# Kernel tuning notes

Measured on AMD Instinct MI355X. Metric: run time of the kernel, lower is better.

Reference implementation:

```python
import jax, jax.numpy as jnp
import numpy as np

B = 2097152  # number of Gaussians


def setup_inputs() -> dict:
    key = jax.random.key(0)
    k1, k2, k3, k4, k5, k6 = jax.random.split(key, 6)
    return {
        "loc1": jax.random.normal(k1, (B, 3), dtype=jnp.float32),
        "scale1": jax.random.uniform(k2, (B, 3), dtype=jnp.float32),
        "rot_matrix1": jax.random.normal(k3, (B, 3, 3), dtype=jnp.float32),
        "loc2": jax.random.normal(k4, (B, 3), dtype=jnp.float32),
        "scale2": jax.random.uniform(k5, (B, 3), dtype=jnp.float32),
        "rot_matrix2": jax.random.normal(k6, (B, 3, 3), dtype=jnp.float32),
    }


def reference(loc1, scale1, rot_matrix1, loc2, scale2, rot_matrix2):
    # ||mu1 - mu2||^2  -> (B,)
    loc_diff2 = jnp.sum((loc1 - loc2) ** 2, axis=-1)

    # cov2 = R2 diag(scale2) R2^T  -> (B,3,3)
    cov2 = jnp.einsum("bij,bj,bkj->bik", rot_matrix2, scale2, rot_matrix2)
    # cov2 rotated into frame of Gaussian 1: R1^T cov2 R1  -> (B,3,3)
    cov2_R1 = jnp.einsum("bji,bjk,bkl->bil", rot_matrix1, cov2, rot_matrix1)

    # E = diag(sqrt(s1)) cov2_R1 diag(sqrt(s1)), then symmetrize
    s1_sqrt = jnp.sqrt(scale1)  # (B,3)
    E = s1_sqrt[:, :, None] * cov2_R1 * s1_sqrt[:, None, :]
    E = (E + jnp.swapaxes(E, 1, 2)) * 0.5

    # trace of matrix sqrt via eigenvalues: sum (lambda^2)^(1/4) = sum |lambda|^(1/2)
    E_eig = jnp.linalg.eigvalsh(E)  # (B,3)
    E_sqrt_trace = jnp.sum(jnp.sqrt(jnp.sqrt(E_eig ** 2)), axis=-1)

    cov_wasserstein = jnp.sum(scale1, axis=-1) + jnp.sum(scale2, axis=-1) - 2.0 * E_sqrt_trace
    cov_wasserstein = jnp.maximum(cov_wasserstein, 0.0)
    return jnp.sqrt(loc_diff2 + cov_wasserstein)
```

## Files before the change

kernel.cpp:

```cpp
#include <hip/hip_runtime.h>
#include <math.h>

#define BLK  256
#define GRID 2048

struct F3 { float x, y, z; };

__device__ __forceinline__ F3 ldF3(const float* p) {
    F3 r; r.x = p[0]; r.y = p[1]; r.z = p[2]; return r;
}

__device__ __forceinline__ float compute_elem(
    const F3 L1, const F3 L2, const F3 S1, const F3 S2,
    const F3 r1a, const F3 r1b, const F3 r1c,
    const F3 r2a, const F3 r2b, const F3 r2c)
{
    const float dx = L1.x - L2.x, dy = L1.y - L2.y, dz = L1.z - L2.z;
    const float loc_diff2 = dx * dx + dy * dy + dz * dz;

    const float s1a = S1.x, s1b = S1.y, s1c = S1.z;
    const float s2a = S2.x, s2b = S2.y, s2c = S2.z;

    const float R1[9] = {r1a.x, r1a.y, r1a.z, r1b.x, r1b.y, r1b.z, r1c.x, r1c.y, r1c.z};
    const float R2[9] = {r2a.x, r2a.y, r2a.z, r2b.x, r2b.y, r2b.z, r2c.x, r2c.y, r2c.z};

    const float m00 = s2a * R2[0] * R2[0] + s2b * R2[1] * R2[1] + s2c * R2[2] * R2[2];
    const float m01 = s2a * R2[0] * R2[3] + s2b * R2[1] * R2[4] + s2c * R2[2] * R2[5];
    const float m02 = s2a * R2[0] * R2[6] + s2b * R2[1] * R2[7] + s2c * R2[2] * R2[8];
    const float m11 = s2a * R2[3] * R2[3] + s2b * R2[4] * R2[4] + s2c * R2[5] * R2[5];
    const float m12 = s2a * R2[3] * R2[6] + s2b * R2[4] * R2[7] + s2c * R2[5] * R2[8];
    const float m22 = s2a * R2[6] * R2[6] + s2b * R2[7] * R2[7] + s2c * R2[8] * R2[8];

    float A[9];
    A[0] = m00 * R1[0] + m01 * R1[3] + m02 * R1[6];
    A[1] = m00 * R1[1] + m01 * R1[4] + m02 * R1[7];
    A[2] = m00 * R1[2] + m01 * R1[5] + m02 * R1[8];
    A[3] = m01 * R1[0] + m11 * R1[3] + m12 * R1[6];
    A[4] = m01 * R1[1] + m11 * R1[4] + m12 * R1[7];
    A[5] = m01 * R1[2] + m11 * R1[5] + m12 * R1[8];
    A[6] = m02 * R1[0] + m12 * R1[3] + m22 * R1[6];
    A[7] = m02 * R1[1] + m12 * R1[4] + m22 * R1[7];
    A[8] = m02 * R1[2] + m12 * R1[5] + m22 * R1[8];

    float T[9];
    T[0] = R1[0] * A[0] + R1[3] * A[3] + R1[6] * A[6];
    T[1] = R1[0] * A[1] + R1[3] * A[4] + R1[6] * A[7];
    T[2] = R1[0] * A[2] + R1[3] * A[5] + R1[6] * A[8];
    T[3] = R1[1] * A[0] + R1[4] * A[3] + R1[7] * A[6];
    T[4] = R1[1] * A[1] + R1[4] * A[4] + R1[7] * A[7];
    T[5] = R1[1] * A[2] + R1[4] * A[5] + R1[7] * A[8];
    T[6] = R1[2] * A[0] + R1[5] * A[3] + R1[8] * A[6];
    T[7] = R1[2] * A[1] + R1[5] * A[4] + R1[8] * A[7];
    T[8] = R1[2] * A[2] + R1[5] * A[5] + R1[8] * A[8];

    const float sq0 = __builtin_amdgcn_sqrtf(s1a);
    const float sq1 = __builtin_amdgcn_sqrtf(s1b);
    const float sq2 = __builtin_amdgcn_sqrtf(s1c);
    const float e00 = s1a * T[0];
    const float e11 = s1b * T[4];
    const float e22 = s1c * T[8];
    const float e01 = 0.5f * sq0 * sq1 * (T[1] + T[3]);
    const float e02 = 0.5f * sq0 * sq2 * (T[2] + T[6]);
    const float e12 = 0.5f * sq1 * sq2 * (T[5] + T[7]);

    const float q  = (e00 + e11 + e22) * (1.0f / 3.0f);
    const float p1 = e01 * e01 + e02 * e02 + e12 * e12;
    const float d0 = e00 - q, d1 = e11 - q, d2 = e22 - q;
    const float p2 = d0 * d0 + d1 * d1 + d2 * d2 + 2.0f * p1;

    float trace_sqrt;
    if (p2 > 1e-24f) {
        const float p   = __builtin_amdgcn_sqrtf(p2 * (1.0f / 6.0f));
        const float inv = __builtin_amdgcn_rcpf(p);
        const float b00 = d0 * inv, b11 = d1 * inv, b22 = d2 * inv;
        const float b01 = e01 * inv, b02 = e02 * inv, b12 = e12 * inv;
        float detB = b00 * (b11 * b22 - b12 * b12)
                   - b01 * (b01 * b22 - b12 * b02)
                   + b02 * (b01 * b12 - b11 * b02);
        float r = 0.5f * detB;
        r = fminf(fmaxf(r, -1.0f), 1.0f);

        const float ax = fabsf(r);
        const float z  = __builtin_amdgcn_sqrtf(1.0f - ax);
        const float w  = z * (1.5707288f + ax * (-0.2121144f
                           + ax * (0.0742610f + ax * (-0.0187293f))));
        const float ac = (r >= 0.0f) ? w : (3.14159265358979f - w);

        const float phi = ac * (1.0f / 3.0f);
        const float c   = __cosf(phi);
        const float s   = __sinf(phi);
        const float twop = 2.0f * p;
        const float eig1 = q + twop * c;
        const float eig3 = q + twop * (-0.5f * c - 0.86602540378f * s);
        const float eig2 = 3.0f * q - eig1 - eig3;
        trace_sqrt = __builtin_amdgcn_sqrtf(fabsf(eig1))
                   + __builtin_amdgcn_sqrtf(fabsf(eig2))
                   + __builtin_amdgcn_sqrtf(fabsf(eig3));
    } else {
        trace_sqrt = 3.0f * __builtin_amdgcn_sqrtf(fabsf(q));
    }

    float cov_w = (s1a + s1b + s1c) + (s2a + s2b + s2c) - 2.0f * trace_sqrt;
    cov_w = fmaxf(cov_w, 0.0f);
    return __builtin_amdgcn_sqrtf(loc_diff2 + cov_w);
}

__global__ __launch_bounds__(BLK, 8) void wasserstein_kernel(
    const float* __restrict__ loc1,   const float* __restrict__ scale1,
    const float* __restrict__ rot1,   const float* __restrict__ loc2,
    const float* __restrict__ scale2, const float* __restrict__ rot2,
    float* __restrict__ out, int B)
{
    const long long stride = (long long)GRID * BLK;
    const long long start  = (long long)blockIdx.x * BLK + threadIdx.x;

    for (long long i = start; i < B; i += stride) {
        const F3 L1  = ldF3(loc1   + i * 3);
        const F3 L2  = ldF3(loc2   + i * 3);
        const F3 S1  = ldF3(scale1 + i * 3);
        const F3 S2  = ldF3(scale2 + i * 3);
        const F3 r1a = ldF3(rot1 + i * 9);
        const F3 r1b = ldF3(rot1 + i * 9 + 3);
        const F3 r1c = ldF3(rot1 + i * 9 + 6);
        const F3 r2a = ldF3(rot2 + i * 9);
        const F3 r2b = ldF3(rot2 + i * 9 + 3);
        const F3 r2c = ldF3(rot2 + i * 9 + 6);

        out[i] = compute_elem(L1, L2, S1, S2, r1a, r1b, r1c, r2a, r2b, r2c);
    }
}

extern "C" void kernel_launch(void* const* d_in, const int* in_sizes, int n_in,
                              void* d_out, int out_size, void* d_ws, size_t ws_size,
                              hipStream_t stream) {
    const float* loc1   = (const float*)d_in[0];
    const float* scale1 = (const float*)d_in[1];
    const float* rot1   = (const float*)d_in[2];
    const float* loc2   = (const float*)d_in[3];
    const float* scale2 = (const float*)d_in[4];
    const float* rot2   = (const float*)d_in[5];
    float* out = (float*)d_out;

    const int B = in_sizes[0] / 3;

    wasserstein_kernel<<<GRID, BLK, 0, stream>>>(loc1, scale1, rot1,
                                                 loc2, scale2, rot2, out, B);
}
```

Before: 242.6 us.

## Software-pipeline loads with double-buffered inline-asm global loads and vmcnt waits

Replaces the grid-stride loop with a fully unrolled, double-buffered pipeline. Each thread handles 8 elements. While the current element is computed, the next batch is already in flight through inline-asm global loads using dwordx2/x4 widths, with explicit s_waitcnt vmcnt gating and 32-bit offsets. The goal is to hide memory latency and cut load instruction count in a bandwidth-bound kernel. The cost is higher register pressure (launch bounds drop to 4) and a fast path specialised to B == GRID*BLK*8, with a generic fallback kernel for other sizes.

```diff
diff --git a/kernel.cpp b/kernel.cpp
--- a/kernel.cpp
+++ b/kernel.cpp
@@ -1,28 +1,62 @@
 #include <hip/hip_runtime.h>
 #include <math.h>
 
-#define BLK  256
-#define GRID 2048
-
-struct F3 { float x, y, z; };
-
-__device__ __forceinline__ F3 ldF3(const float* p) {
-    F3 r; r.x = p[0]; r.y = p[1]; r.z = p[2]; return r;
-}
-
-__device__ __forceinline__ float compute_elem(
-    const F3 L1, const F3 L2, const F3 S1, const F3 S2,
-    const F3 r1a, const F3 r1b, const F3 r1c,
-    const F3 r2a, const F3 r2b, const F3 r2c)
-{
-    const float dx = L1.x - L2.x, dy = L1.y - L2.y, dz = L1.z - L2.z;
+#define BLK    256
+#define GRID   1024
+#define EPT    8
+#define STRIDE (GRID * BLK)
+
+typedef float v2f __attribute__((ext_vector_type(2)));
+typedef float v4f __attribute__((ext_vector_type(4)));
+
+struct Pay {
+    v2f l1a; float l1z;
+    v2f l2a; float l2z;
+    v2f s1a; float s1z;
+    v2f s2a; float s2z;
+    v4f r1a; v4f r1b; float r1c;
+    v4f r2a; v4f r2b; float r2c;
+};
+
+__device__ __forceinline__ void load_batch(Pay& p, unsigned off12, unsigned off36,
+    const float* loc1, const float* loc2, const float* sc1, const float* sc2,
+    const float* rot1, const float* rot2)
+{
+    asm volatile("global_load_dwordx2 %0, %1, %2"           : "=v"(p.l1a) : "v"(off12), "s"(loc1));
+    asm volatile("global_load_dword   %0, %1, %2 offset:8"  : "=v"(p.l1z) : "v"(off12), "s"(loc1));
+    asm volatile("global_load_dwordx2 %0, %1, %2"           : "=v"(p.l2a) : "v"(off12), "s"(loc2));
+    asm volatile("global_load_dword   %0, %1, %2 offset:8"  : "=v"(p.l2z) : "v"(off12), "s"(loc2));
+    asm volatile("global_load_dwordx2 %0, %1, %2"           : "=v"(p.s1a) : "v"(off12), "s"(sc1));
+    asm volatile("global_load_dword   %0, %1, %2 offset:8"  : "=v"(p.s1z) : "v"(off12), "s"(sc1));
+    asm volatile("global_load_dwordx2 %0, %1, %2"           : "=v"(p.s2a) : "v"(off12), "s"(sc2));
+    asm volatile("global_load_dword   %0, %1, %2 offset:8"  : "=v"(p.s2z) : "v"(off12), "s"(sc2));
+    asm volatile("global_load_dwordx4 %0, %1, %2"           : "=v"(p.r1a) : "v"(off36), "s"(rot1));
+    asm volatile("global_load_dwordx4 %0, %1, %2 offset:16" : "=v"(p.r1b) : "v"(off36), "s"(rot1));
+    asm volatile("global_load_dword   %0, %1, %2 offset:32" : "=v"(p.r1c) : "v"(off36), "s"(rot1));
+    asm volatile("global_load_dwordx4 %0, %1, %2"           : "=v"(p.r2a) : "v"(off36), "s"(rot2));
+    asm volatile("global_load_dwordx4 %0, %1, %2 offset:16" : "=v"(p.r2b) : "v"(off36), "s"(rot2));
+    asm volatile("global_load_dword   %0, %1, %2 offset:32" : "=v"(p.r2c) : "v"(off36), "s"(rot2));
+}
+
+#define WAITV(N)  asm volatile("s_waitcnt vmcnt(" #N ")" ::: "memory")
+#define SBAR()    __builtin_amdgcn_sched_barrier(0)
+
+__device__ __forceinline__ void store_val(float v, unsigned off4, float* out) {
+    asm volatile("global_store_dword %0, %1, %2" :: "v"(off4), "v"(v), "s"(out) : "memory");
+}
+
+__device__ __forceinline__ float compute_pay(const Pay& e)
+{
+    const float dx = e.l1a.x - e.l2a.x, dy = e.l1a.y - e.l2a.y, dz = e.l1z - e.l2z;
     const float loc_diff2 = dx * dx + dy * dy + dz * dz;
 
-    const float s1a = S1.x, s1b = S1.y, s1c = S1.z;
-    const float s2a = S2.x, s2b = S2.y, s2c = S2.z;
-
-    const float R1[9] = {r1a.x, r1a.y, r1a.z, r1b.x, r1b.y, r1b.z, r1c.x, r1c.y, r1c.z};
-    const float R2[9] = {r2a.x, r2a.y, r2a.z, r2b.x, r2b.y, r2b.z, r2c.x, r2c.y, r2c.z};
+    const float s1a = e.s1a.x, s1b = e.s1a.y, s1c = e.s1z;
+    const float s2a = e.s2a.x, s2b = e.s2a.y, s2c = e.s2z;
+
+    const float R1[9] = {e.r1a.x, e.r1a.y, e.r1a.z, e.r1a.w,
+                         e.r1b.x, e.r1b.y, e.r1b.z, e.r1b.w, e.r1c};
+    const float R2[9] = {e.r2a.x, e.r2a.y, e.r2a.z, e.r2a.w,
+                         e.r2b.x, e.r2b.y, e.r2b.z, e.r2b.w, e.r2c};
 
     const float m00 = s2a * R2[0] * R2[0] + s2b * R2[1] * R2[1] + s2c * R2[2] * R2[2];
     const float m01 = s2a * R2[0] * R2[3] + s2b * R2[1] * R2[4] + s2c * R2[2] * R2[5];
@@ -105,29 +139,69 @@
     return __builtin_amdgcn_sqrtf(loc_diff2 + cov_w);
 }
 
-__global__ __launch_bounds__(BLK, 8) void wasserstein_kernel(
+__global__ __launch_bounds__(BLK, 4) void wasserstein_pipe(
+    const float* __restrict__ loc1,   const float* __restrict__ scale1,
+    const float* __restrict__ rot1,   const float* __restrict__ loc2,
+    const float* __restrict__ scale2, const float* __restrict__ rot2,
+    float* __restrict__ out)
+{
+    const unsigned i0 = blockIdx.x * BLK + threadIdx.x;
+    unsigned offL12 = i0 * 12u, offL36 = i0 * 36u;
+    unsigned offS4  = i0 * 4u;
+    const unsigned D12 = STRIDE * 12u, D36 = STRIDE * 36u, D4 = STRIDE * 4u;
+
+    Pay A, B;
+    load_batch(A, offL12, offL36, loc1, loc2, scale1, scale2, rot1, rot2);
+    offL12 += D12; offL36 += D36;
+    load_batch(B, offL12, offL36, loc1, loc2, scale1, scale2, rot1, rot2);
+    offL12 += D12; offL36 += D36;
+
+#define STEP_LOAD(BUF)                                                        \
+    WAITV(15); SBAR();                                                        \
+    store_val(compute_pay(BUF), offS4, out); offS4 += D4;                     \
+    load_batch(BUF, offL12, offL36, loc1, loc2, scale1, scale2, rot1, rot2);  \
+    offL12 += D12; offL36 += D36;
+
+    WAITV(14); SBAR();
+    store_val(compute_pay(A), offS4, out); offS4 += D4;
+    load_batch(A, offL12, offL36, loc1, loc2, scale1, scale2, rot1, rot2);
+    offL12 += D12; offL36 += D36;
+
+    STEP_LOAD(B)
+    STEP_LOAD(A)
+    STEP_LOAD(B)
+    STEP_LOAD(A)
+    STEP_LOAD(B)
+
+    WAITV(15); SBAR();
+    store_val(compute_pay(A), offS4, out); offS4 += D4;
+
+    WAITV(1); SBAR();
+    store_val(compute_pay(B), offS4, out);
+#undef STEP_LOAD
+}
+
+__global__ void wasserstein_simple(
     const float* __restrict__ loc1,   const float* __restrict__ scale1,
     const float* __restrict__ rot1,   const float* __restrict__ loc2,
     const float* __restrict__ scale2, const float* __restrict__ rot2,
     float* __restrict__ out, int B)
 {
-    const long long stride = (long long)GRID * BLK;
-    const long long start  = (long long)blockIdx.x * BLK + threadIdx.x;
-
-    for (long long i = start; i < B; i += stride) {
-        const F3 L1  = ldF3(loc1   + i * 3);
-        const F3 L2  = ldF3(loc2   + i * 3);
-        const F3 S1  = ldF3(scale1 + i * 3);
-        const F3 S2  = ldF3(scale2 + i * 3);
-        const F3 r1a = ldF3(rot1 + i * 9);
-        const F3 r1b = ldF3(rot1 + i * 9 + 3);
-        const F3 r1c = ldF3(rot1 + i * 9 + 6);
-        const F3 r2a = ldF3(rot2 + i * 9);
-        const F3 r2b = ldF3(rot2 + i * 9 + 3);
-        const F3 r2c = ldF3(rot2 + i * 9 + 6);
-
-        out[i] = compute_elem(L1, L2, S1, S2, r1a, r1b, r1c, r2a, r2b, r2c);
-    }
+    long long i = (long long)blockIdx.x * blockDim.x + threadIdx.x;
+    if (i >= B) return;
+    Pay e;
+    const float* p;
+    p = loc1 + i * 3;   e.l1a.x = p[0]; e.l1a.y = p[1]; e.l1z = p[2];
+    p = loc2 + i * 3;   e.l2a.x = p[0]; e.l2a.y = p[1]; e.l2z = p[2];
+    p = scale1 + i * 3; e.s1a.x = p[0]; e.s1a.y = p[1]; e.s1z = p[2];
+    p = scale2 + i * 3; e.s2a.x = p[0]; e.s2a.y = p[1]; e.s2z = p[2];
+    p = rot1 + i * 9;
+    e.r1a.x = p[0]; e.r1a.y = p[1]; e.r1a.z = p[2]; e.r1a.w = p[3];
+    e.r1b.x = p[4]; e.r1b.y = p[5]; e.r1b.z = p[6]; e.r1b.w = p[7]; e.r1c = p[8];
+    p = rot2 + i * 9;
+    e.r2a.x = p[0]; e.r2a.y = p[1]; e.r2a.z = p[2]; e.r2a.w = p[3];
+    e.r2b.x = p[4]; e.r2b.y = p[5]; e.r2b.z = p[6]; e.r2b.w = p[7]; e.r2c = p[8];
+    out[i] = compute_pay(e);
 }
 
 extern "C" void kernel_launch(void* const* d_in, const int* in_sizes, int n_in,
@@ -143,6 +217,12 @@
 
     const int B = in_sizes[0] / 3;
 
-    wasserstein_kernel<<<GRID, BLK, 0, stream>>>(loc1, scale1, rot1,
-                                                 loc2, scale2, rot2, out, B);
-}
+    if (B == STRIDE * EPT) {
+        wasserstein_pipe<<<GRID, BLK, 0, stream>>>(loc1, scale1, rot1,
+                                                   loc2, scale2, rot2, out);
+    } else {
+        const int grid = (B + BLK - 1) / BLK;
+        wasserstein_simple<<<grid, BLK, 0, stream>>>(loc1, scale1, rot1,
+                                                     loc2, scale2, rot2, out, B);
+    }
+}
```

Measured after the change: 241.3 us. Within noise of the previous version (-0.5%).
